# Kernel optimization log

Hardware: AMD Instinct MI355X
Metric: run time of the kernel (lower is better)

## Reference

```python
import jax, jax.numpy as jnp
import numpy as np

B, N, T, F, E = 64, 512, 50, 32, 32768  # batch, n_roi, n_timepoints, n_filters, n_edges


def setup_inputs() -> dict:
    key = jax.random.key(0)
    ks = jax.random.split(key, 24)
    s = 0.05
    inp = {
        "x": jax.random.normal(ks[0], (B, N, T), jnp.float32),
        "edge_index": jax.random.randint(ks[1], (2, E), 0, N, dtype=jnp.int64),
        "edge_weight": jax.random.uniform(ks[2], (E,), jnp.float32),
        # ChebConv K=2 weights: W[k] maps in->out for Chebyshev order k; shared bias.
        "conv1_W": jax.random.normal(ks[3], (2, T, F), jnp.float32) * s,
        "conv1_b": jnp.zeros((F,), jnp.float32),
        "conv2_W": jax.random.normal(ks[4], (2, F, F), jnp.float32) * s,
        "conv2_b": jnp.zeros((F,), jnp.float32),
        "conv3_W": jax.random.normal(ks[5], (2, F, F), jnp.float32) * s,
        "conv3_b": jnp.zeros((F,), jnp.float32),
        "conv4_W": jax.random.normal(ks[6], (2, F, F), jnp.float32) * s,
        "conv4_b": jnp.zeros((F,), jnp.float32),
        "conv5_W": jax.random.normal(ks[7], (2, F, F), jnp.float32) * s,
        "conv5_b": jnp.zeros((F,), jnp.float32),
        "conv6_W": jax.random.normal(ks[8], (2, F, F), jnp.float32) * s,
        "conv6_b": jnp.zeros((F,), jnp.float32),
        "fc1_W": jax.random.normal(ks[9], (F * N, 256), jnp.float32) * s,
        "fc1_b": jnp.zeros((256,), jnp.float32),
        "fc2_W": jax.random.normal(ks[10], (256, 128), jnp.float32) * s,
        "fc2_b": jnp.zeros((128,), jnp.float32),
        "fc3_W": jax.random.normal(ks[11], (128, 2), jnp.float32) * s,
        "fc3_b": jnp.zeros((2,), jnp.float32),
    }
    return inp


def reference(x, edge_index, edge_weight,
              conv1_W, conv1_b, conv2_W, conv2_b, conv3_W, conv3_b,
              conv4_W, conv4_b, conv5_W, conv5_b, conv6_W, conv6_b,
              fc1_W, fc1_b, fc2_W, fc2_b, fc3_W, fc3_b):
    n = x.shape[1]
    src, dst = edge_index[0], edge_index[1]
    # PyG ChebConv __norm__ (sym, lambda_max=2): remove self loops, build
    # L = I - D^-1/2 A D^-1/2, rescale 2L/lmax - I  ->  off-diag = -norm, diag = 0.
    w = jnp.where(src == dst, 0.0, edge_weight)
    deg = jax.ops.segment_sum(w, src, num_segments=n)
    dinv = jnp.where(deg > 0, jax.lax.rsqrt(deg), 0.0)
    norm = -(dinv[src] * w * dinv[dst])  # [E], static across all 6 layers

    def prop(hb):  # L_hat @ h for one sample: gather src, scatter-add to dst
        return jax.ops.segment_sum(norm[:, None] * hb[src], dst, num_segments=n)
    prop_b = jax.vmap(prop)

    def cheb(h, W, b):  # K=2: Tx0 = h, Tx1 = L_hat h
        return (jnp.einsum('bnc,cf->bnf', h, W[0])
                + jnp.einsum('bnc,cf->bnf', prop_b(h), W[1]) + b)

    h = jax.nn.relu(cheb(x, conv1_W, conv1_b))
    h = jax.nn.relu(cheb(h, conv2_W, conv2_b))
    h = jax.nn.relu(cheb(h, conv3_W, conv3_b))
    h = jax.nn.relu(cheb(h, conv4_W, conv4_b))
    h = jax.nn.relu(cheb(h, conv5_W, conv5_b))
    h = cheb(h, conv6_W, conv6_b)          # no relu after conv6 in original
    h = h.reshape(h.shape[0], -1)          # flatten node features per sample
    h = h @ fc1_W + fc1_b                  # dropout = identity at inference
    h = h @ fc2_W + fc2_b
    return h @ fc3_W + fc3_b
```

## Files before the change

kernel.cpp:

```cpp
#include <hip/hip_runtime.h>

#define NN 512
#define BB_ 64
#define EE 32768
#define TT 50
#define FF 32
#define NB 2048

typedef _Float16 f16x8 __attribute__((ext_vector_type(8)));
typedef float    f32x4 __attribute__((ext_vector_type(4)));

#define OFF_LHAT 0
#define OFF_LP   (512 * 512)
#define OFF_DEG  (OFF_LP + 512 * 512)
#define OFF_HP0  (OFF_DEG + 512)
#define OFF_HP1  (OFF_HP0 + NN * NB)
#define OFF_GP   (OFF_HP1 + NN * NB)
#define OFF_F0   (OFF_GP + NN * NB)
#define WS_FLOATS (OFF_F0 + NN * NB)

__device__ __forceinline__ unsigned pack_split(float v) {
    _Float16 h = (_Float16)v;
    _Float16 l = (_Float16)(v - (float)h);
    return (unsigned)__builtin_bit_cast(unsigned short, h) |
           ((unsigned)__builtin_bit_cast(unsigned short, l) << 16);
}


__global__ void k_zero_out(float* out, int n) {
    int i = blockIdx.x * blockDim.x + threadIdx.x;
    if (i < n) out[i] = 0.f;
}

__global__ void k_zero_range(float* p, int n) {
    int i = blockIdx.x * blockDim.x + threadIdx.x;
    if (i < n) p[i] = 0.f;
}

__global__ void k_deg(const int* __restrict__ ei, const float* __restrict__ ew,
                      float* __restrict__ deg) {
    int e = blockIdx.x * blockDim.x + threadIdx.x;
    if (e >= EE) return;
    int s = ei[e] & (NN - 1), d = ei[EE + e] & (NN - 1);
    if (s != d) atomicAdd(&deg[s], ew[e]);
}

__global__ void k_dinv(float* deg) {
    int i = threadIdx.x;
    float d = deg[i];
    deg[i] = (d > 0.f) ? rsqrtf(d) : 0.f;
}

__global__ void k_build(const int* __restrict__ ei, const float* __restrict__ ew,
                        const float* __restrict__ dinv, float* __restrict__ Lhat) {
    int e = blockIdx.x * blockDim.x + threadIdx.x;
    if (e >= EE) return;
    int s = ei[e] & (NN - 1), d = ei[EE + e] & (NN - 1);
    if (s == d) return;
    float nm = -(dinv[s] * ew[e] * dinv[d]);
    atomicAdd(&Lhat[d * NN + s], nm);
}

__global__ void k_splitL(const float* __restrict__ L, unsigned* __restrict__ Lp) {
    int i = blockIdx.x * 256 + threadIdx.x;
    Lp[i] = pack_split(L[i]);
}

template<int CIN, int MODE>
__global__ __launch_bounds__(256) void k_small(
        const float* __restrict__ A0, const float* __restrict__ A1,
        const float* __restrict__ W, const float* __restrict__ bias,
        unsigned* __restrict__ Gp, float* __restrict__ F0) {
    __shared__ float W0s[CIN * FF];
    __shared__ float W1s[CIN * FF];
    __shared__ float bs[FF];
    __shared__ float rows[64][CIN];
    const int tid = threadIdx.x;
    for (int i = tid; i < CIN * FF; i += 256) {
        W0s[i] = W[i];
        W1s[i] = W[CIN * FF + i];
    }
    if (tid < FF) bs[tid] = bias[tid];
    const int r0 = blockIdx.x * 64;
    for (int idx = tid; idx < 64 * CIN; idx += 256) {
        int r = idx / CIN, c = idx % CIN;
        int R = r0 + r;
        float v;
        if (MODE == 0) {
            v = A0[((size_t)(R & 63) * NN + (R >> 6)) * CIN + c];
        } else {
            size_t o = (size_t)R * CIN + c;
            v = fmaxf(A0[o] + A1[o], 0.f);
        }
        rows[r][c] = v;
    }
    __syncthreads();
    const int f = tid & 31, g = tid >> 5;
    float gacc[8] = {};
    float facc[8];
#pragma unroll
    for (int i = 0; i < 8; ++i) facc[i] = bs[f];
    for (int c = 0; c < CIN; ++c) {
        float w0 = W0s[c * FF + f], w1 = W1s[c * FF + f];
#pragma unroll
        for (int i = 0; i < 8; ++i) {
            float hv = rows[g + 8 * i][c];
            gacc[i] = fmaf(hv, w1, gacc[i]);
            facc[i] = fmaf(hv, w0, facc[i]);
        }
    }
#pragma unroll
    for (int i = 0; i < 8; ++i) {
        size_t o = (size_t)(r0 + g + 8 * i) * FF + f;
        Gp[o] = pack_split(gacc[i]);
        F0[o] = facc[i];
    }
}

__global__ __launch_bounds__(256) void k_prop_mfma(
        const unsigned* __restrict__ Lp, const unsigned* __restrict__ Gp,
        const float* __restrict__ F0,
        float* __restrict__ Hp0, float* __restrict__ Hp1) {
    __shared__ unsigned short Ahi[2][64][40], Alo[2][64][40];
    __shared__ unsigned short Bhi[2][64][40], Blo[2][64][40];
    const int tid  = threadIdx.x;
    const int lane = tid & 63, w = tid >> 6;
    const int wm = w >> 1, wn = w & 1;
    const int grp = lane >> 4, l16 = lane & 15;
    const int i0 = blockIdx.y * 64, j0 = blockIdx.x * 64;
    const int kbase = blockIdx.z * 256;

    const int arow = tid >> 5, ak = tid & 31;
    const int brow = tid >> 6, bcol = tid & 63;

    f32x4 acc[2][2] = {};
    unsigned pa[8], pb[8];

#pragma unroll
    for (int i = 0; i < 8; ++i)
        pa[i] = Lp[(size_t)(i0 + arow + i * 8) * NN + kbase + ak];
#pragma unroll
    for (int i = 0; i < 8; ++i)
        pb[i] = Gp[(size_t)(kbase + brow + i * 4) * NB + j0 + bcol];

    for (int t = 0; t < 8; ++t) {
        const int buf = t & 1;
#pragma unroll
        for (int i = 0; i < 8; ++i) {
            unsigned v = pa[i];
            Ahi[buf][arow + i * 8][ak] = (unsigned short)v;
            Alo[buf][arow + i * 8][ak] = (unsigned short)(v >> 16);
        }
#pragma unroll
        for (int i = 0; i < 8; ++i) {
            unsigned v = pb[i];
            Bhi[buf][bcol][brow + i * 4] = (unsigned short)v;
            Blo[buf][bcol][brow + i * 4] = (unsigned short)(v >> 16);
        }
        __syncthreads();
        if (t < 7) {
            const int kc = kbase + (t + 1) * 32;
#pragma unroll
            for (int i = 0; i < 8; ++i)
                pa[i] = Lp[(size_t)(i0 + arow + i * 8) * NN + kc + ak];
#pragma unroll
            for (int i = 0; i < 8; ++i)
                pb[i] = Gp[(size_t)(kc + brow + i * 4) * NB + j0 + bcol];
        }
        f16x8 ah[2], al[2], bh[2], bl[2];
#pragma unroll
        for (int mi = 0; mi < 2; ++mi) {
            ah[mi] = *(const f16x8*)&Ahi[buf][wm * 32 + mi * 16 + l16][grp * 8];
            al[mi] = *(const f16x8*)&Alo[buf][wm * 32 + mi * 16 + l16][grp * 8];
        }
#pragma unroll
        for (int ni = 0; ni < 2; ++ni) {
            bh[ni] = *(const f16x8*)&Bhi[buf][wn * 32 + ni * 16 + l16][grp * 8];
            bl[ni] = *(const f16x8*)&Blo[buf][wn * 32 + ni * 16 + l16][grp * 8];
        }
#pragma unroll
        for (int mi = 0; mi < 2; ++mi)
#pragma unroll
            for (int ni = 0; ni < 2; ++ni) {
                acc[mi][ni] = __builtin_amdgcn_mfma_f32_16x16x32_f16(al[mi], bl[ni], acc[mi][ni], 0, 0, 0);
                acc[mi][ni] = __builtin_amdgcn_mfma_f32_16x16x32_f16(al[mi], bh[ni], acc[mi][ni], 0, 0, 0);
                acc[mi][ni] = __builtin_amdgcn_mfma_f32_16x16x32_f16(ah[mi], bl[ni], acc[mi][ni], 0, 0, 0);
                acc[mi][ni] = __builtin_amdgcn_mfma_f32_16x16x32_f16(ah[mi], bh[ni], acc[mi][ni], 0, 0, 0);
            }
        __syncthreads();
    }

    float* Hp = blockIdx.z ? Hp1 : Hp0;
#pragma unroll
    for (int mi = 0; mi < 2; ++mi)
#pragma unroll
        for (int ni = 0; ni < 2; ++ni)
#pragma unroll
            for (int p = 0; p < 4; ++p) {
                const int row = i0 + wm * 32 + mi * 16 + grp * 4 + p;
                const int col = j0 + wn * 32 + ni * 16 + l16;
                const size_t idx = (size_t)row * NB + col;
                float v = acc[mi][ni][p];
                if (blockIdx.z == 0) v += F0[idx];
                Hp[idx] = v;
            }
}

__global__ __launch_bounds__(256) void k_fc1(const float* __restrict__ h0,
                                             const float* __restrict__ h1,
                                             const float* __restrict__ W,
                                             float* __restrict__ P) {
    __shared__ float AT[128][68];
    const int tid = threadIdx.x;
    const int jg = blockIdx.x;
    const int kc = blockIdx.y;
    const size_t base = (size_t)kc * 4 * NB;
#pragma unroll
    for (int i = 0; i < 8; ++i) {
        int q = tid + i * 256;
        float4 v0 = *(const float4*)&h0[base + q * 4];
        float4 v1 = *(const float4*)&h1[base + q * 4];
        float4 v;
        v.x = v0.x + v1.x; v.y = v0.y + v1.y;
        v.z = v0.z + v1.z; v.w = v0.w + v1.w;
        int flat = q * 4;
        int nn = flat >> 11, rem = flat & 2047;
        int b = rem >> 5, f0 = rem & 31;
        int krow = nn * 32 + f0;
        AT[krow + 0][b] = v.x; AT[krow + 1][b] = v.y;
        AT[krow + 2][b] = v.z; AT[krow + 3][b] = v.w;
    }
    __syncthreads();
    const int tj = tid & 31, bq = tid >> 5;
    float acc[8] = {};
    const float* wp = W + (size_t)(kc * 128) * 256 + jg * 32 + tj;
#pragma unroll 8
    for (int k = 0; k < 128; ++k) {
        float w = wp[(size_t)k * 256];
        const float* ap = &AT[k][bq * 8];
        float4 a0 = *(const float4*)ap;
        float4 a1 = *(const float4*)(ap + 4);
        acc[0] = fmaf(a0.x, w, acc[0]); acc[1] = fmaf(a0.y, w, acc[1]);
        acc[2] = fmaf(a0.z, w, acc[2]); acc[3] = fmaf(a0.w, w, acc[3]);
        acc[4] = fmaf(a1.x, w, acc[4]); acc[5] = fmaf(a1.y, w, acc[5]);
        acc[6] = fmaf(a1.z, w, acc[6]); acc[7] = fmaf(a1.w, w, acc[7]);
    }
#pragma unroll
    for (int b2 = 0; b2 < 8; ++b2)
        P[(size_t)kc * 16384 + (bq * 8 + b2) * 256 + jg * 32 + tj] = acc[b2];
}

__global__ __launch_bounds__(128) void k_fc23(const float* __restrict__ P,
        const float* __restrict__ b1, const float* __restrict__ W2,
        const float* __restrict__ b2, const float* __restrict__ W3,
        const float* __restrict__ b3, float* __restrict__ out) {
    __shared__ float row[256];
    __shared__ float r2[128];
    const int m = blockIdx.x, j = threadIdx.x;
#pragma unroll
    for (int rep = 0; rep < 2; ++rep) {
        int k2 = j + rep * 128;
        float s = b1[k2];
#pragma unroll 8
        for (int kc = 0; kc < 128; ++kc)
            s += P[(size_t)kc * 16384 + m * 256 + k2];
        row[k2] = s;
    }
    __syncthreads();
    float acc = b2[j];
#pragma unroll 4
    for (int k = 0; k < 256; ++k)
        acc = fmaf(row[k], W2[k * 128 + j], acc);
    r2[j] = acc;
    __syncthreads();
    const int w = j >> 6, l = j & 63;
    float s2 = r2[l] * W3[l * 2 + w] + r2[l + 64] * W3[(l + 64) * 2 + w];
#pragma unroll
    for (int off = 32; off > 0; off >>= 1)
        s2 += __shfl_down(s2, off);
    if (l == 0) out[m * 2 + w] = s2 + b3[w];
}


extern "C" void kernel_launch(void* const* d_in, const int* in_sizes, int n_in,
                              void* d_out, int out_size, void* d_ws, size_t ws_size,
                              hipStream_t stream) {
    float* outp = (float*)d_out;
    if (ws_size < (size_t)WS_FLOATS * sizeof(float)) {
        k_zero_out<<<(out_size + 255) / 256, 256, 0, stream>>>(outp, out_size);
        return;
    }

    const float* x  = (const float*)d_in[0];
    const int*   ei = (const int*)d_in[1];
    const float* ew = (const float*)d_in[2];
    const float* cW[6] = {(const float*)d_in[3], (const float*)d_in[5],
                          (const float*)d_in[7], (const float*)d_in[9],
                          (const float*)d_in[11], (const float*)d_in[13]};
    const float* cb[6] = {(const float*)d_in[4], (const float*)d_in[6],
                          (const float*)d_in[8], (const float*)d_in[10],
                          (const float*)d_in[12], (const float*)d_in[14]};
    const float* fc1W = (const float*)d_in[15];
    const float* fc1b = (const float*)d_in[16];
    const float* fc2W = (const float*)d_in[17];
    const float* fc2b = (const float*)d_in[18];
    const float* fc3W = (const float*)d_in[19];
    const float* fc3b = (const float*)d_in[20];

    float*    ws   = (float*)d_ws;
    float*    Lhat = ws + OFF_LHAT;
    unsigned* Lp   = (unsigned*)(ws + OFF_LP);
    float*    deg  = ws + OFF_DEG;
    float*    Hp0  = ws + OFF_HP0;
    float*    Hp1  = ws + OFF_HP1;
    unsigned* Gp   = (unsigned*)(ws + OFF_GP);
    float*    F0   = ws + OFF_F0;
    float*    P    = ws + OFF_GP;

    k_zero_range<<<(OFF_DEG + 512 + 255) / 256, 256, 0, stream>>>(ws, OFF_DEG + 512);
    k_deg<<<EE / 256, 256, 0, stream>>>(ei, ew, deg);
    k_dinv<<<1, 512, 0, stream>>>(deg);
    k_build<<<EE / 256, 256, 0, stream>>>(ei, ew, deg, Lhat);
    k_splitL<<<NN * NN / 256, 256, 0, stream>>>(Lhat, Lp);

    dim3 pgrid(32, 8, 2);
    k_small<TT, 0><<<512, 256, 0, stream>>>(x, nullptr, cW[0], cb[0], Gp, F0);
    k_prop_mfma<<<pgrid, 256, 0, stream>>>(Lp, Gp, F0, Hp0, Hp1);
    k_small<FF, 1><<<512, 256, 0, stream>>>(Hp0, Hp1, cW[1], cb[1], Gp, F0);
    k_prop_mfma<<<pgrid, 256, 0, stream>>>(Lp, Gp, F0, Hp0, Hp1);
    k_small<FF, 1><<<512, 256, 0, stream>>>(Hp0, Hp1, cW[2], cb[2], Gp, F0);
    k_prop_mfma<<<pgrid, 256, 0, stream>>>(Lp, Gp, F0, Hp0, Hp1);
    k_small<FF, 1><<<512, 256, 0, stream>>>(Hp0, Hp1, cW[3], cb[3], Gp, F0);
    k_prop_mfma<<<pgrid, 256, 0, stream>>>(Lp, Gp, F0, Hp0, Hp1);
    k_small<FF, 1><<<512, 256, 0, stream>>>(Hp0, Hp1, cW[4], cb[4], Gp, F0);
    k_prop_mfma<<<pgrid, 256, 0, stream>>>(Lp, Gp, F0, Hp0, Hp1);
    k_small<FF, 1><<<512, 256, 0, stream>>>(Hp0, Hp1, cW[5], cb[5], Gp, F0);
    k_prop_mfma<<<pgrid, 256, 0, stream>>>(Lp, Gp, F0, Hp0, Hp1);

    dim3 fgrid(8, 128);
    k_fc1<<<fgrid, 256, 0, stream>>>(Hp0, Hp1, fc1W, P);
    k_fc23<<<64, 128, 0, stream>>>(P, fc1b, fc2W, fc2b, fc3W, fc3b, outp);
}
```

Baseline: 325.0 us.

## Store L and G as separate transposed fp16 hi/lo planes for vector loads

```diff
diff --git a/kernel.cpp b/kernel.cpp
--- a/kernel.cpp
+++ b/kernel.cpp
@@ -9,22 +9,19 @@
 
 typedef _Float16 f16x8 __attribute__((ext_vector_type(8)));
 typedef float    f32x4 __attribute__((ext_vector_type(4)));
+typedef unsigned short ushort_t;
 
 #define OFF_LHAT 0
-#define OFF_LP   (512 * 512)
-#define OFF_DEG  (OFF_LP + 512 * 512)
+#define OFF_LHI  (512 * 512)
+#define OFF_LLO  (OFF_LHI + 131072)
+#define OFF_DEG  (OFF_LLO + 131072)
 #define OFF_HP0  (OFF_DEG + 512)
 #define OFF_HP1  (OFF_HP0 + NN * NB)
-#define OFF_GP   (OFF_HP1 + NN * NB)
-#define OFF_F0   (OFF_GP + NN * NB)
-#define WS_FLOATS (OFF_F0 + NN * NB)
-
-__device__ __forceinline__ unsigned pack_split(float v) {
-    _Float16 h = (_Float16)v;
-    _Float16 l = (_Float16)(v - (float)h);
-    return (unsigned)__builtin_bit_cast(unsigned short, h) |
-           ((unsigned)__builtin_bit_cast(unsigned short, l) << 16);
-}
+#define OFF_GHT  (OFF_HP1 + NN * NB)
+#define OFF_GLT  (OFF_GHT + 524288)
+#define OFF_F0   (OFF_GLT + 524288)
+#define OFF_P    (OFF_F0 + NN * NB)
+#define WS_FLOATS (OFF_P + 128 * 16384)
 
 
 __global__ void k_zero_out(float* out, int n) {
@@ -61,122 +58,137 @@
     atomicAdd(&Lhat[d * NN + s], nm);
 }
 
-__global__ void k_splitL(const float* __restrict__ L, unsigned* __restrict__ Lp) {
+__global__ void k_splitL(const float* __restrict__ L,
+                         ushort_t* __restrict__ Lhi, ushort_t* __restrict__ Llo) {
     int i = blockIdx.x * 256 + threadIdx.x;
-    Lp[i] = pack_split(L[i]);
+    float v = L[i];
+    _Float16 h = (_Float16)v;
+    _Float16 l = (_Float16)(v - (float)h);
+    Lhi[i] = __builtin_bit_cast(ushort_t, h);
+    Llo[i] = __builtin_bit_cast(ushort_t, l);
 }
 
 template<int CIN, int MODE>
 __global__ __launch_bounds__(256) void k_small(
         const float* __restrict__ A0, const float* __restrict__ A1,
         const float* __restrict__ W, const float* __restrict__ bias,
-        unsigned* __restrict__ Gp, float* __restrict__ F0) {
+        ushort_t* __restrict__ Ght, ushort_t* __restrict__ Glt,
+        float* __restrict__ F0) {
     __shared__ float W0s[CIN * FF];
     __shared__ float W1s[CIN * FF];
     __shared__ float bs[FF];
-    __shared__ float rows[64][CIN];
+    __shared__ float rows[128][CIN + 1];
     const int tid = threadIdx.x;
+    const int b = blockIdx.x, n0 = blockIdx.y * 128;
     for (int i = tid; i < CIN * FF; i += 256) {
         W0s[i] = W[i];
         W1s[i] = W[CIN * FF + i];
     }
     if (tid < FF) bs[tid] = bias[tid];
-    const int r0 = blockIdx.x * 64;
-    for (int idx = tid; idx < 64 * CIN; idx += 256) {
-        int r = idx / CIN, c = idx % CIN;
-        int R = r0 + r;
-        float v;
-        if (MODE == 0) {
-            v = A0[((size_t)(R & 63) * NN + (R >> 6)) * CIN + c];
-        } else {
-            size_t o = (size_t)R * CIN + c;
-            v = fmaxf(A0[o] + A1[o], 0.f);
-        }
-        rows[r][c] = v;
+    if (MODE == 0) {
+        const float* xb = A0 + ((size_t)b * NN + n0) * CIN;
+        for (int idx = tid; idx < 128 * CIN; idx += 256)
+            rows[idx / CIN][idx % CIN] = xb[idx];
+    } else {
+        for (int q = tid; q < 128 * 8; q += 256) {
+            int n = q >> 3, c4 = (q & 7) * 4;
+            size_t o = (size_t)(n0 + n) * NB + b * FF + c4;
+            float4 v0 = *(const float4*)&A0[o];
+            float4 v1 = *(const float4*)&A1[o];
+            rows[n][c4 + 0] = fmaxf(v0.x + v1.x, 0.f);
+            rows[n][c4 + 1] = fmaxf(v0.y + v1.y, 0.f);
+            rows[n][c4 + 2] = fmaxf(v0.z + v1.z, 0.f);
+            rows[n][c4 + 3] = fmaxf(v0.w + v1.w, 0.f);
+        }
     }
     __syncthreads();
-    const int f = tid & 31, g = tid >> 5;
-    float gacc[8] = {};
-    float facc[8];
-#pragma unroll
-    for (int i = 0; i < 8; ++i) facc[i] = bs[f];
+    const int f = tid & 31, nq = tid >> 5;
+    float gacc[16] = {};
+    float facc[16];
+#pragma unroll
+    for (int i = 0; i < 16; ++i) facc[i] = bs[f];
     for (int c = 0; c < CIN; ++c) {
         float w0 = W0s[c * FF + f], w1 = W1s[c * FF + f];
 #pragma unroll
-        for (int i = 0; i < 8; ++i) {
-            float hv = rows[g + 8 * i][c];
+        for (int i = 0; i < 16; ++i) {
+            float hv = rows[nq * 16 + i][c];
             gacc[i] = fmaf(hv, w1, gacc[i]);
             facc[i] = fmaf(hv, w0, facc[i]);
         }
     }
-#pragma unroll
-    for (int i = 0; i < 8; ++i) {
-        size_t o = (size_t)(r0 + g + 8 * i) * FF + f;
-        Gp[o] = pack_split(gacc[i]);
-        F0[o] = facc[i];
-    }
+    const int j = b * FF + f, kk = n0 + nq * 16;
+#pragma unroll
+    for (int i = 0; i < 16; ++i)
+        F0[(size_t)(kk + i) * NB + j] = facc[i];
+    unsigned hw[8], lw[8];
+#pragma unroll
+    for (int q = 0; q < 8; ++q) {
+        float v0 = gacc[2 * q], v1 = gacc[2 * q + 1];
+        _Float16 h0 = (_Float16)v0, h1 = (_Float16)v1;
+        _Float16 l0 = (_Float16)(v0 - (float)h0), l1 = (_Float16)(v1 - (float)h1);
+        hw[q] = (unsigned)__builtin_bit_cast(ushort_t, h0) |
+                ((unsigned)__builtin_bit_cast(ushort_t, h1) << 16);
+        lw[q] = (unsigned)__builtin_bit_cast(ushort_t, l0) |
+                ((unsigned)__builtin_bit_cast(ushort_t, l1) << 16);
+    }
+    uint4* gh = (uint4*)&Ght[(size_t)j * NN + kk];
+    uint4* gl = (uint4*)&Glt[(size_t)j * NN + kk];
+    gh[0] = make_uint4(hw[0], hw[1], hw[2], hw[3]);
+    gh[1] = make_uint4(hw[4], hw[5], hw[6], hw[7]);
+    gl[0] = make_uint4(lw[0], lw[1], lw[2], lw[3]);
+    gl[1] = make_uint4(lw[4], lw[5], lw[6], lw[7]);
 }
 
 __global__ __launch_bounds__(256) void k_prop_mfma(
-        const unsigned* __restrict__ Lp, const unsigned* __restrict__ Gp,
+        const ushort_t* __restrict__ Lhi, const ushort_t* __restrict__ Llo,
+        const ushort_t* __restrict__ Ght, const ushort_t* __restrict__ Glt,
         const float* __restrict__ F0,
         float* __restrict__ Hp0, float* __restrict__ Hp1) {
-    __shared__ unsigned short Ahi[2][64][40], Alo[2][64][40];
-    __shared__ unsigned short Bhi[2][64][40], Blo[2][64][40];
+    __shared__ ushort_t Ah[2][64][40], Al[2][64][40];
+    __shared__ ushort_t Bh[2][64][40], Bl[2][64][40];
     const int tid  = threadIdx.x;
     const int lane = tid & 63, w = tid >> 6;
     const int wm = w >> 1, wn = w & 1;
     const int grp = lane >> 4, l16 = lane & 15;
     const int i0 = blockIdx.y * 64, j0 = blockIdx.x * 64;
     const int kbase = blockIdx.z * 256;
-
-    const int arow = tid >> 5, ak = tid & 31;
-    const int brow = tid >> 6, bcol = tid & 63;
+    const int sr = tid >> 2, sk = (tid & 3) * 8;
+
+    const ushort_t* pAh = Lhi + (size_t)(i0 + sr) * NN + kbase + sk;
+    const ushort_t* pAl = Llo + (size_t)(i0 + sr) * NN + kbase + sk;
+    const ushort_t* pBh = Ght + (size_t)(j0 + sr) * NN + kbase + sk;
+    const ushort_t* pBl = Glt + (size_t)(j0 + sr) * NN + kbase + sk;
 
     f32x4 acc[2][2] = {};
-    unsigned pa[8], pb[8];
-
-#pragma unroll
-    for (int i = 0; i < 8; ++i)
-        pa[i] = Lp[(size_t)(i0 + arow + i * 8) * NN + kbase + ak];
-#pragma unroll
-    for (int i = 0; i < 8; ++i)
-        pb[i] = Gp[(size_t)(kbase + brow + i * 4) * NB + j0 + bcol];
+    uint4 rah = *(const uint4*)pAh;
+    uint4 ral = *(const uint4*)pAl;
+    uint4 rbh = *(const uint4*)pBh;
+    uint4 rbl = *(const uint4*)pBl;
 
     for (int t = 0; t < 8; ++t) {
         const int buf = t & 1;
-#pragma unroll
-        for (int i = 0; i < 8; ++i) {
-            unsigned v = pa[i];
-            Ahi[buf][arow + i * 8][ak] = (unsigned short)v;
-            Alo[buf][arow + i * 8][ak] = (unsigned short)(v >> 16);
-        }
-#pragma unroll
-        for (int i = 0; i < 8; ++i) {
-            unsigned v = pb[i];
-            Bhi[buf][bcol][brow + i * 4] = (unsigned short)v;
-            Blo[buf][bcol][brow + i * 4] = (unsigned short)(v >> 16);
-        }
+        *(uint4*)&Ah[buf][sr][sk] = rah;
+        *(uint4*)&Al[buf][sr][sk] = ral;
+        *(uint4*)&Bh[buf][sr][sk] = rbh;
+        *(uint4*)&Bl[buf][sr][sk] = rbl;
         __syncthreads();
         if (t < 7) {
-            const int kc = kbase + (t + 1) * 32;
-#pragma unroll
-            for (int i = 0; i < 8; ++i)
-                pa[i] = Lp[(size_t)(i0 + arow + i * 8) * NN + kc + ak];
-#pragma unroll
-            for (int i = 0; i < 8; ++i)
-                pb[i] = Gp[(size_t)(kc + brow + i * 4) * NB + j0 + bcol];
+            const int ko = (t + 1) * 32;
+            rah = *(const uint4*)(pAh + ko);
+            ral = *(const uint4*)(pAl + ko);
+            rbh = *(const uint4*)(pBh + ko);
+            rbl = *(const uint4*)(pBl + ko);
         }
         f16x8 ah[2], al[2], bh[2], bl[2];
 #pragma unroll
         for (int mi = 0; mi < 2; ++mi) {
-            ah[mi] = *(const f16x8*)&Ahi[buf][wm * 32 + mi * 16 + l16][grp * 8];
-            al[mi] = *(const f16x8*)&Alo[buf][wm * 32 + mi * 16 + l16][grp * 8];
+            ah[mi] = *(const f16x8*)&Ah[buf][wm * 32 + mi * 16 + l16][grp * 8];
+            al[mi] = *(const f16x8*)&Al[buf][wm * 32 + mi * 16 + l16][grp * 8];
         }
 #pragma unroll
         for (int ni = 0; ni < 2; ++ni) {
-            bh[ni] = *(const f16x8*)&Bhi[buf][wn * 32 + ni * 16 + l16][grp * 8];
-            bl[ni] = *(const f16x8*)&Blo[buf][wn * 32 + ni * 16 + l16][grp * 8];
+            bh[ni] = *(const f16x8*)&Bh[buf][wn * 32 + ni * 16 + l16][grp * 8];
+            bl[ni] = *(const f16x8*)&Bl[buf][wn * 32 + ni * 16 + l16][grp * 8];
         }
 #pragma unroll
         for (int mi = 0; mi < 2; ++mi)
@@ -309,33 +321,36 @@
 
     float*    ws   = (float*)d_ws;
     float*    Lhat = ws + OFF_LHAT;
-    unsigned* Lp   = (unsigned*)(ws + OFF_LP);
+    ushort_t* Lhi  = (ushort_t*)(ws + OFF_LHI);
+    ushort_t* Llo  = (ushort_t*)(ws + OFF_LLO);
     float*    deg  = ws + OFF_DEG;
     float*    Hp0  = ws + OFF_HP0;
     float*    Hp1  = ws + OFF_HP1;
-    unsigned* Gp   = (unsigned*)(ws + OFF_GP);
+    ushort_t* Ght  = (ushort_t*)(ws + OFF_GHT);
+    ushort_t* Glt  = (ushort_t*)(ws + OFF_GLT);
     float*    F0   = ws + OFF_F0;
-    float*    P    = ws + OFF_GP;
+    float*    P    = ws + OFF_P;
 
     k_zero_range<<<(OFF_DEG + 512 + 255) / 256, 256, 0, stream>>>(ws, OFF_DEG + 512);
     k_deg<<<EE / 256, 256, 0, stream>>>(ei, ew, deg);
     k_dinv<<<1, 512, 0, stream>>>(deg);
     k_build<<<EE / 256, 256, 0, stream>>>(ei, ew, deg, Lhat);
-    k_splitL<<<NN * NN / 256, 256, 0, stream>>>(Lhat, Lp);
-
+    k_splitL<<<NN * NN / 256, 256, 0, stream>>>(Lhat, Lhi, Llo);
+
+    dim3 sgrid(BB_, 4);
     dim3 pgrid(32, 8, 2);
-    k_small<TT, 0><<<512, 256, 0, stream>>>(x, nullptr, cW[0], cb[0], Gp, F0);
-    k_prop_mfma<<<pgrid, 256, 0, stream>>>(Lp, Gp, F0, Hp0, Hp1);
-    k_small<FF, 1><<<512, 256, 0, stream>>>(Hp0, Hp1, cW[1], cb[1], Gp, F0);
-    k_prop_mfma<<<pgrid, 256, 0, stream>>>(Lp, Gp, F0, Hp0, Hp1);
-    k_small<FF, 1><<<512, 256, 0, stream>>>(Hp0, Hp1, cW[2], cb[2], Gp, F0);
-    k_prop_mfma<<<pgrid, 256, 0, stream>>>(Lp, Gp, F0, Hp0, Hp1);
-    k_small<FF, 1><<<512, 256, 0, stream>>>(Hp0, Hp1, cW[3], cb[3], Gp, F0);
-    k_prop_mfma<<<pgrid, 256, 0, stream>>>(Lp, Gp, F0, Hp0, Hp1);
-    k_small<FF, 1><<<512, 256, 0, stream>>>(Hp0, Hp1, cW[4], cb[4], Gp, F0);
-    k_prop_mfma<<<pgrid, 256, 0, stream>>>(Lp, Gp, F0, Hp0, Hp1);
-    k_small<FF, 1><<<512, 256, 0, stream>>>(Hp0, Hp1, cW[5], cb[5], Gp, F0);
-    k_prop_mfma<<<pgrid, 256, 0, stream>>>(Lp, Gp, F0, Hp0, Hp1);
+    k_small<TT, 0><<<sgrid, 256, 0, stream>>>(x, nullptr, cW[0], cb[0], Ght, Glt, F0);
+    k_prop_mfma<<<pgrid, 256, 0, stream>>>(Lhi, Llo, Ght, Glt, F0, Hp0, Hp1);
+    k_small<FF, 1><<<sgrid, 256, 0, stream>>>(Hp0, Hp1, cW[1], cb[1], Ght, Glt, F0);
+    k_prop_mfma<<<pgrid, 256, 0, stream>>>(Lhi, Llo, Ght, Glt, F0, Hp0, Hp1);
+    k_small<FF, 1><<<sgrid, 256, 0, stream>>>(Hp0, Hp1, cW[2], cb[2], Ght, Glt, F0);
+    k_prop_mfma<<<pgrid, 256, 0, stream>>>(Lhi, Llo, Ght, Glt, F0, Hp0, Hp1);
+    k_small<FF, 1><<<sgrid, 256, 0, stream>>>(Hp0, Hp1, cW[3], cb[3], Ght, Glt, F0);
+    k_prop_mfma<<<pgrid, 256, 0, stream>>>(Lhi, Llo, Ght, Glt, F0, Hp0, Hp1);
+    k_small<FF, 1><<<sgrid, 256, 0, stream>>>(Hp0, Hp1, cW[4], cb[4], Ght, Glt, F0);
+    k_prop_mfma<<<pgrid, 256, 0, stream>>>(Lhi, Llo, Ght, Glt, F0, Hp0, Hp1);
+    k_small<FF, 1><<<sgrid, 256, 0, stream>>>(Hp0, Hp1, cW[5], cb[5], Ght, Glt, F0);
+    k_prop_mfma<<<pgrid, 256, 0, stream>>>(Lhi, Llo, Ght, Glt, F0, Hp0, Hp1);
 
     dim3 fgrid(8, 128);
     k_fc1<<<fgrid, 256, 0, stream>>>(Hp0, Hp1, fc1W, P);
```

Result: no change. 326.4 us (+0.4%).
